# Kernel tuning notes

Hardware: AMD Instinct MI355X
Metric: run time of the kernel (lower is better)

The kernel has to match this reference:

```python
import jax, jax.numpy as jnp
import numpy as np

N_BLOCKS = 12   # grid rows == cols
D = 256         # per-block feature size (small -> memory-bound)
BATCH = 8192    # samples per block

# Deterministic block-sparse pattern: block (i, j) is active iff (i - j) % 3 == 0.
_mask = np.array([[(i - j) % 3 == 0 for j in range(N_BLOCKS)] for i in range(N_BLOCKS)])
_I, _J = np.nonzero(_mask)  # 48 active blocks
N_ACTIVE = _I.shape[0]


def setup_inputs() -> dict:
    key = jax.random.key(0)
    k1, k2, k3 = jax.random.split(key, 3)
    X = jax.random.normal(k1, (N_BLOCKS, BATCH, D), dtype=jnp.float32)
    # One Linear(D, D) per active block: weight [K, D_in, D_out], bias [K, D_out]
    W = jax.random.normal(k2, (N_ACTIVE, D, D), dtype=jnp.float32) / np.sqrt(D).astype(np.float32)
    b = jax.random.normal(k3, (N_ACTIVE, D), dtype=jnp.float32) * 0.01
    i_idx = jnp.asarray(_I, dtype=jnp.int32)  # output-row index of each active block
    j_idx = jnpim if False else jnp.asarray(_J, dtype=jnp.int32)  # input-col index of each active block
    return {"X": X, "W": W, "b": b, "i_idx": i_idx, "j_idx": j_idx}


def reference(X, W, b, i_idx, j_idx):
    # Gather the input block feeding each active sub-module: [K, BATCH, D]
    Xg = X[j_idx]
    # Apply each block's Linear in one batched contraction: [K, BATCH, D]
    h = jnp.einsum('kbi,kio->kbo', Xg, W) + b[:, None, :]
    # Sum block outputs into their output rows (the '+' combiner / safe_sum):
    # rows with no active block get an all-zero output, matching the zero-vector semantics.
    y = jax.ops.segment_sum(h, i_idx, num_segments=N_BLOCKS)  # [N_BLOCKS, BATCH, D]
    return y
```

## Files before the change

### kernel.cpp

```cpp
#include <hip/hip_runtime.h>

#define N_BLOCKS 12
#define D 256
#define BATCH 8192

typedef __attribute__((ext_vector_type(8))) short bf16x8;
typedef __attribute__((ext_vector_type(4))) float f32x4;

__device__ __forceinline__ unsigned short f2bf(float f) {
  unsigned int u = __float_as_uint(f);
  u += 0x7fffu + ((u >> 16) & 1u);
  return (unsigned short)(u >> 16);
}

__device__ __forceinline__ void gld16(const unsigned short* g, unsigned short* l) {
  __builtin_amdgcn_global_load_lds(
      (const __attribute__((address_space(1))) unsigned int*)g,
      (__attribute__((address_space(3))) unsigned int*)l,
      16, 0, 0);
}

__global__ void cvt_x(const float* __restrict__ X, unsigned short* __restrict__ Xb) {
  const long long t = (long long)blockIdx.x * 256 + threadIdx.x;
  const long long base = t * 8;
  const float4 v0 = *(const float4*)(X + base);
  const float4 v1 = *(const float4*)(X + base + 4);
  uint4 r;
  r.x = (unsigned)f2bf(v0.x) | ((unsigned)f2bf(v0.y) << 16);
  r.y = (unsigned)f2bf(v0.z) | ((unsigned)f2bf(v0.w) << 16);
  r.z = (unsigned)f2bf(v1.x) | ((unsigned)f2bf(v1.y) << 16);
  r.w = (unsigned)f2bf(v1.z) | ((unsigned)f2bf(v1.w) << 16);
  *(uint4*)(Xb + base) = r;
}

__global__ void cvt_w(const float* __restrict__ W, unsigned short* __restrict__ Wt) {
  __shared__ unsigned short tile[32][33];
  const int k  = blockIdx.x >> 6;
  const int t  = blockIdx.x & 63;
  const int ti = t >> 3;
  const int tj = t & 7;
  const float* Wk = W + (long long)k * D * D;
  unsigned short* Wtk = Wt + (long long)k * D * D;
  const int lx = threadIdx.x & 31, ly = threadIdx.x >> 5;
  #pragma unroll
  for (int r = 0; r < 4; ++r) {
    const int i = ti * 32 + ly + r * 8;
    const int o = tj * 32 + lx;
    tile[ly + r * 8][lx] = f2bf(Wk[i * D + o]);
  }
  __syncthreads();
  #pragma unroll
  for (int r = 0; r < 4; ++r) {
    const int o = tj * 32 + ly + r * 8;
    const int i = ti * 32 + lx;
    Wtk[o * D + i] = tile[lx][ly + r * 8];
  }
}

__launch_bounds__(256)
__global__ void bs_gemm(const unsigned short* __restrict__ Xb,
                        const unsigned short* __restrict__ Wt,
                        const float* __restrict__ bias,
                        const int* __restrict__ i_idx,
                        const int* __restrict__ j_idx,
                        int nact,
                        float* __restrict__ Y) {
  __shared__ unsigned short sA[128 * 32];
  __shared__ unsigned short sB[128 * 32];

  const int bid = blockIdx.x;
  const int i   = bid >> 7;
  const int rem = bid & 127;
  const int bm  = rem >> 1;
  const int bn  = rem & 1;

  int ks[8], js[8], nk = 0;
  for (int k = 0; k < nact; ++k)
    if (i_idx[k] == i && nk < 8) { ks[nk] = k; js[nk] = j_idx[k]; ++nk; }

  const int tid  = threadIdx.x;
  const int wave = tid >> 6;
  const int lane = tid & 63;
  const int wr   = wave >> 1, wc = wave & 1;

  const int L1 = tid, L2 = tid + 256;
  const int r1 = L1 >> 2, c1 = (L1 & 3) ^ ((r1 >> 1) & 3);
  const int r2 = L2 >> 2, c2 = (L2 & 3) ^ ((r2 >> 1) & 3);
  const int g1 = r1 * D + c1 * 8;
  const int g2 = r2 * D + c2 * 8;
  unsigned short* lA1 = sA + L1 * 8;
  unsigned short* lA2 = sA + L2 * 8;
  unsigned short* lB1 = sB + L1 * 8;
  unsigned short* lB2 = sB + L2 * 8;

  const int q      = lane >> 4;
  const int a_row  = wr * 64 + (lane & 15);
  const int b_row  = wc * 64 + (lane & 15);
  const int a_sw   = (q ^ ((a_row >> 1) & 3)) * 8;
  const int b_sw   = (q ^ ((b_row >> 1) & 3)) * 8;

  f32x4 acc[4][4] = {};

  for (int t = 0; t < nk; ++t) {
    const unsigned short* Ab = Xb + ((long long)js[t] * BATCH + bm * 128) * D;
    const unsigned short* Bb = Wt + ((long long)ks[t] * D + bn * 128) * D;
    #pragma unroll
    for (int d0 = 0; d0 < D; d0 += 32) {
      gld16(Ab + g1 + d0, lA1);
      gld16(Ab + g2 + d0, lA2);
      gld16(Bb + g1 + d0, lB1);
      gld16(Bb + g2 + d0, lB2);
      __syncthreads();

      bf16x8 aF[4], bF[4];
      #pragma unroll
      for (int mt = 0; mt < 4; ++mt)
        aF[mt] = *(const bf16x8*)(sA + (a_row + mt * 16) * 32 + a_sw);
      #pragma unroll
      for (int nt = 0; nt < 4; ++nt)
        bF[nt] = *(const bf16x8*)(sB + (b_row + nt * 16) * 32 + b_sw);
      #pragma unroll
      for (int mt = 0; mt < 4; ++mt)
        #pragma unroll
        for (int nt = 0; nt < 4; ++nt)
          acc[mt][nt] = __builtin_amdgcn_mfma_f32_16x16x32_bf16(
              aF[mt], bF[nt], acc[mt][nt], 0, 0, 0);
      __syncthreads();
    }
  }

  float* Yb = Y + (long long)i * BATCH * D;
  const int m0 = bm * 128 + wr * 64 + (q * 4);
  const int n0 = bn * 128 + wc * 64 + (lane & 15);
  float bsum[4];
  #pragma unroll
  for (int nt = 0; nt < 4; ++nt) {
    float s = 0.f;
    for (int t = 0; t < nk; ++t) s += bias[ks[t] * D + n0 + nt * 16];
    bsum[nt] = s;
  }
  #pragma unroll
  for (int nt = 0; nt < 4; ++nt) {
    #pragma unroll
    for (int mt = 0; mt < 4; ++mt)
      #pragma unroll
      for (int r = 0; r < 4; ++r)
        Yb[(long long)(m0 + mt * 16 + r) * D + (n0 + nt * 16)] = acc[mt][nt][r] + bsum[nt];
  }
}

extern "C" void kernel_launch(void* const* d_in, const int* in_sizes, int n_in,
                              void* d_out, int out_size, void* d_ws, size_t ws_size,
                              hipStream_t stream) {
  const float* X = (const float*)d_in[0];
  const float* W = (const float*)d_in[1];
  const float* b = (const float*)d_in[2];
  const int* i_idx = (const int*)d_in[3];
  const int* j_idx = (const int*)d_in[4];
  float* Y = (float*)d_out;
  const int nact = in_sizes[3];

  unsigned short* Xb = (unsigned short*)d_ws;
  unsigned short* Wt = (unsigned short*)((char*)d_ws + (size_t)N_BLOCKS * BATCH * D * 2);

  cvt_x<<<(N_BLOCKS * BATCH * D) / (256 * 8), 256, 0, stream>>>(X, Xb);
  cvt_w<<<nact * 64, 256, 0, stream>>>(W, Wt);
  bs_gemm<<<N_BLOCKS * 64 * 2, 256, 0, stream>>>(Xb, Wt, b, i_idx, j_idx, nact, Y);
}
```

Before: 274.0 us.

## Double-buffer LDS tiles and flatten block-sparse K loop into one pipelined loop

Replaces the single-buffered LDS staging with a two-stage ping-pong buffer, so global-to-LDS loads for the next K slice are issued before the MFMAs on the current one. The per-active-block loop and the inner D loop are merged into one fully unrolled 32-step loop that assumes exactly four active blocks per output row. The XOR swizzle on LDS addresses is dropped, which may bring back bank conflicts on fragment reads. It also hardcodes nk=4, so rows with fewer active blocks would read invalid pointers.

```diff
diff --git a/kernel.cpp b/kernel.cpp
--- a/kernel.cpp
+++ b/kernel.cpp
@@ -65,8 +65,7 @@
                         const int* __restrict__ j_idx,
                         int nact,
                         float* __restrict__ Y) {
-  __shared__ unsigned short sA[128 * 32];
-  __shared__ unsigned short sB[128 * 32];
+  __shared__ unsigned short sm[4 * 4096];
 
   const int bid = blockIdx.x;
   const int i   = bid >> 7;
@@ -74,59 +73,73 @@
   const int bm  = rem >> 1;
   const int bn  = rem & 1;
 
-  int ks[8], js[8], nk = 0;
+  int ks[4], js[4], nk = 0;
   for (int k = 0; k < nact; ++k)
-    if (i_idx[k] == i && nk < 8) { ks[nk] = k; js[nk] = j_idx[k]; ++nk; }
+    if (i_idx[k] == i && nk < 4) { ks[nk] = k; js[nk] = j_idx[k]; ++nk; }
 
   const int tid  = threadIdx.x;
   const int wave = tid >> 6;
   const int lane = tid & 63;
   const int wr   = wave >> 1, wc = wave & 1;
 
-  const int L1 = tid, L2 = tid + 256;
-  const int r1 = L1 >> 2, c1 = (L1 & 3) ^ ((r1 >> 1) & 3);
-  const int r2 = L2 >> 2, c2 = (L2 & 3) ^ ((r2 >> 1) & 3);
-  const int g1 = r1 * D + c1 * 8;
-  const int g2 = r2 * D + c2 * 8;
-  unsigned short* lA1 = sA + L1 * 8;
-  unsigned short* lA2 = sA + L2 * 8;
-  unsigned short* lB1 = sB + L1 * 8;
-  unsigned short* lB2 = sB + L2 * 8;
+  const int g_off = (tid >> 2) * D + (tid & 3) * 8;
+
+  const unsigned short* At[4];
+  const unsigned short* Bt[4];
+  #pragma unroll
+  for (int t = 0; t < 4; ++t) {
+    At[t] = Xb + ((long long)js[t] * BATCH + bm * 128) * D + g_off;
+    Bt[t] = Wt + ((long long)ks[t] * D + bn * 128) * D + g_off;
+  }
 
   const int q      = lane >> 4;
+  const int frag_k = q * 8;
   const int a_row  = wr * 64 + (lane & 15);
   const int b_row  = wc * 64 + (lane & 15);
-  const int a_sw   = (q ^ ((a_row >> 1) & 3)) * 8;
-  const int b_sw   = (q ^ ((b_row >> 1) & 3)) * 8;
 
   f32x4 acc[4][4] = {};
 
-  for (int t = 0; t < nk; ++t) {
-    const unsigned short* Ab = Xb + ((long long)js[t] * BATCH + bm * 128) * D;
-    const unsigned short* Bb = Wt + ((long long)ks[t] * D + bn * 128) * D;
+  {
+    unsigned short* lA = sm + tid * 8;
+    unsigned short* lB = sm + 2 * 4096 + tid * 8;
+    gld16(At[0], lA);
+    gld16(At[0] + 64 * D, lA + 2048);
+    gld16(Bt[0], lB);
+    gld16(Bt[0] + 64 * D, lB + 2048);
+  }
+
+  #pragma unroll
+  for (int u = 0; u < 32; ++u) {
+    const int p = u & 1;
+    __syncthreads();
+
+    if (u < 31) {
+      const int un = u + 1;
+      const unsigned short* Ab = At[un >> 3] + ((un & 7) << 5);
+      const unsigned short* Bb = Bt[un >> 3] + ((un & 7) << 5);
+      unsigned short* lA = sm + (p ^ 1) * 4096 + tid * 8;
+      unsigned short* lB = sm + (2 + (p ^ 1)) * 4096 + tid * 8;
+      gld16(Ab, lA);
+      gld16(Ab + 64 * D, lA + 2048);
+      gld16(Bb, lB);
+      gld16(Bb + 64 * D, lB + 2048);
+    }
+
+    const unsigned short* sA = sm + p * 4096;
+    const unsigned short* sB = sm + (2 + p) * 4096;
+    bf16x8 aF[4], bF[4];
     #pragma unroll
-    for (int d0 = 0; d0 < D; d0 += 32) {
-      gld16(Ab + g1 + d0, lA1);
-      gld16(Ab + g2 + d0, lA2);
-      gld16(Bb + g1 + d0, lB1);
-      gld16(Bb + g2 + d0, lB2);
-      __syncthreads();
-
-      bf16x8 aF[4], bF[4];
-      #pragma unroll
-      for (int mt = 0; mt < 4; ++mt)
-        aF[mt] = *(const bf16x8*)(sA + (a_row + mt * 16) * 32 + a_sw);
+    for (int mt = 0; mt < 4; ++mt)
+      aF[mt] = *(const bf16x8*)(sA + (a_row + mt * 16) * 32 + frag_k);
+    #pragma unroll
+    for (int nt = 0; nt < 4; ++nt)
+      bF[nt] = *(const bf16x8*)(sB + (b_row + nt * 16) * 32 + frag_k);
+    #pragma unroll
+    for (int mt = 0; mt < 4; ++mt)
       #pragma unroll
       for (int nt = 0; nt < 4; ++nt)
-        bF[nt] = *(const bf16x8*)(sB + (b_row + nt * 16) * 32 + b_sw);
-      #pragma unroll
-      for (int mt = 0; mt < 4; ++mt)
-        #pragma unroll
-        for (int nt = 0; nt < 4; ++nt)
-          acc[mt][nt] = __builtin_amdgcn_mfma_f32_16x16x32_bf16(
-              aF[mt], bF[nt], acc[mt][nt], 0, 0, 0);
-      __syncthreads();
-    }
+        acc[mt][nt] = __builtin_amdgcn_mfma_f32_16x16x32_bf16(
+            aF[mt], bF[nt], acc[mt][nt], 0, 0, 0);
   }
 
   float* Yb = Y + (long long)i * BATCH * D;
```

Result: no change. 271.6 us (-0.9%).
